# Kernel optimization log

Measured on AMD Instinct MI355X. Metric: run time of the kernel, lower is better.

Reference implementation:

```python
import jax, jax.numpy as jnp
import numpy as np

DIM = 1024
HEAD_DIM = 128
NUM_HEADS = 8
T = 8192
ATTN_SCALE = 0.1  # yarn.attn_scale after reset()
RMS_EPS = 1.1920929e-07  # torch F.rms_norm default eps for fp32


def setup_inputs() -> dict:
    key = jax.random.key(0)
    ks = jax.random.split(key, 6)
    x = jax.random.normal(ks[0], (1, T, DIM), jnp.float32)
    qkvo_w = jax.random.normal(ks[1], (4 * DIM, DIM), jnp.float32) * (DIM ** -0.5)
    ve = jax.random.normal(ks[2], (1, T, DIM), jnp.float32)
    sa_lambdas = jnp.array([0.9, 1.1], jnp.float32)
    attn_gate_w = jax.random.normal(ks[3], (NUM_HEADS, 12), jnp.float32) * 0.1
    ve_gate_w = jax.random.normal(ks[4], (NUM_HEADS, 12), jnp.float32) * 0.1
    # YaRN rotary factors, exactly as Yarn.reset()
    n_freq = HEAD_DIM // 4
    ang = (1.0 / 1024.0) ** jnp.linspace(0.0, 1.0, n_freq, dtype=jnp.float32)
    ang = jnp.repeat(ang, 2)                                   # [head_dim//2]
    ang = jnp.concatenate([ang, jnp.zeros(HEAD_DIM // 2, jnp.float32)])
    theta = jnp.arange(T, dtype=jnp.float32)[:, None] * ang[None, :]
    sign = jnp.where(jnp.arange(HEAD_DIM) % 2 == 1, -1.0, 1.0).astype(jnp.float32)
    factor1 = jnp.cos(theta)
    factor2 = jnp.sin(theta) * sign                            # odd lanes negated
    seqlens = jnp.array([0, 2048, 4096, 6144, 8192], jnp.int32)  # cu_seqlens
    return {"x": x, "qkvo_w": qkvo_w, "ve": ve, "sa_lambdas": sa_lambdas,
            "factor1": factor1, "factor2": factor2,
            "attn_gate_w": attn_gate_w, "ve_gate_w": ve_gate_w,
            "seqlens": seqlens, "bm_size": 128, "key_offset": 1}


def _rms_norm(x):
    return x * jax.lax.rsqrt(jnp.mean(x * x, axis=-1, keepdims=True) + RMS_EPS)


def _rotary(x, f1, f2):
    # x: [B, T, H, D]; pairwise flip of adjacent lanes, then f1*x + f2*flip(x)
    xf = x.reshape(*x.shape[:-1], x.shape[-1] // 2, 2)[..., ::-1].reshape(x.shape)
    return f1[None, :x.shape[1], None, :] * x + f2[None, :x.shape[1], None, :] * xf


def _windowed_varlen_attn(q, k, v, seqlens, bs, scale):
    # q,k,v: [T, H, D]; causal sliding window (bs left, 0 right), varlen via cu_seqlens.
    Tt, H, D = q.shape
    nb = Tt // bs
    pad = jnp.zeros((bs, H, D), q.dtype)
    kp = jnp.concatenate([pad, k], axis=0)
    vp = jnp.concatenate([pad, v], axis=0)
    idx = jnp.arange(nb)[:, None] * bs + jnp.arange(2 * bs)[None, :]   # [nb, 2bs] into padded
    kb, vb = kp[idx], vp[idx]                                          # [nb, 2bs, H, D]
    qb = q.reshape(nb, bs, H, D)
    gq = jnp.arange(Tt).reshape(nb, bs)                                # global query idx
    gk = idx - bs                                                      # global key idx (may be <0)
    seg = jnp.searchsorted(seqlens, jnp.arange(Tt), side='right')      # segment id per token
    sq = seg.reshape(nb, bs)
    sk = seg[jnp.clip(gk, 0, Tt - 1)]
    mask = ((gk[:, None, :] >= 0)
            & (gk[:, None, :] <= gq[:, :, None])
            & (gq[:, :, None] - gk[:, None, :] <= bs)
            & (sq[:, :, None] == sk[:, None, :]))                      # [nb, bs, 2bs]
    s = jnp.einsum('nqhd,nkhd->nhqk', qb, kb) * scale
    s = jnp.where(mask[:, None], s, -jnp.inf)
    p = jax.nn.softmax(s, axis=-1)
    return jnp.einsum('nhqk,nkhd->nqhd', p, vb).reshape(Tt, H, D)


def _forward(x, qkvo_w, ve, sa_lambdas, factor1, factor2, attn_gate_w, ve_gate_w,
             seqlens, bm_size, key_offset):
    B, Tt = x.shape[0], x.shape[1]
    H, D = NUM_HEADS, HEAD_DIM
    qkv = x @ (sa_lambdas[0] * qkvo_w[:3 * DIM]).T                    # [B, T, 3*dim]
    qkv = qkv.reshape(B, Tt, 3 * H, D)
    q, k, v = qkv[:, :, :H], qkv[:, :, H:2 * H], qkv[:, :, 2 * H:]
    q, k = _rms_norm(q), _rms_norm(k)
    q, k = _rotary(q, factor1, factor2), _rotary(k, factor1, factor2)
    if key_offset:
        hd2 = D // 2
        k_hi = jnp.concatenate([k[:, :1, :, hd2:], k[:, :-1, :, hd2:]], axis=1)
        k = jnp.concatenate([k[..., :hd2], k_hi], axis=-1)
    ve_gate = 2.0 * jax.nn.sigmoid(x[..., :12] @ ve_gate_w.T).reshape(B, Tt, H, 1)
    v = v + ve_gate * ve.reshape(B, Tt, H, D)
    y = _windowed_varlen_attn(q[0], k[0], v[0], seqlens, bm_size, ATTN_SCALE)
    y = y.reshape(B, Tt, H, D)
    y = y * jax.nn.sigmoid(x[..., :12] @ attn_gate_w.T).reshape(B, Tt, H, 1)
    y = y.reshape(B, Tt, H * D)
    return y @ (sa_lambdas[1] * qkvo_w[3 * DIM:]).T


def reference(x, qkvo_w, ve, sa_lambdas, factor1, factor2, attn_gate_w, ve_gate_w,
              seqlens, bm_size, key_offset):
    return _forward(x, qkvo_w, ve, sa_lambdas, factor1, factor2,
                    attn_gate_w, ve_gate_w, seqlens, bm_size, key_offset)
```

## Files before the change

### kernel.cpp

```cpp
#include <hip/hip_runtime.h>


#define TSEQ 8192
#define DIMM 1024
#define NHEAD 8
#define HD 128
#define ATTN_SCALE 0.1f
#define RMS_EPS 1.1920929e-07f

typedef __bf16 bfx2 __attribute__((ext_vector_type(2)));
typedef __bf16 bfx4 __attribute__((ext_vector_type(4)));
typedef __bf16 bfx8 __attribute__((ext_vector_type(8)));
typedef float f32x4 __attribute__((ext_vector_type(4)));
typedef short s16x4 __attribute__((ext_vector_type(4)));

#define GLDS16(g, l)                                                         \
  __builtin_amdgcn_global_load_lds(                                          \
      (const __attribute__((address_space(1))) void*)(g),                    \
      (__attribute__((address_space(3))) void*)(l), 16, 0, 0)

__device__ __forceinline__ float sig_(float z) { return 1.0f / (1.0f + __expf(-z)); }

__global__ void k_prep(const float4* __restrict__ x, const float4* __restrict__ w,
                       const float* __restrict__ lam, bfx4* __restrict__ xb,
                       bfx4* __restrict__ w1b, bfx4* __restrict__ w2b) {
  const int nx = TSEQ * DIMM / 4;
  const int nw = 4096 * 1024 / 4;
  const float l0 = lam[0], l1 = lam[1];
  int i = blockIdx.x * blockDim.x + threadIdx.x;
  int stride = gridDim.x * blockDim.x;
  for (; i < nx + nw; i += stride) {
    if (i < nx) {
      float4 v = x[i];
      bfx4 o;
      o[0] = (__bf16)v.x; o[1] = (__bf16)v.y; o[2] = (__bf16)v.z; o[3] = (__bf16)v.w;
      xb[i] = o;
    } else {
      int j = i - nx;
      int row = (j * 4) >> 10;
      float s = (row < 3 * DIMM) ? l0 : l1;
      float4 v = w[j];
      bfx4 o;
      o[0] = (__bf16)(s * v.x); o[1] = (__bf16)(s * v.y);
      o[2] = (__bf16)(s * v.z); o[3] = (__bf16)(s * v.w);
      if (row < 3 * DIMM) w1b[j] = o;
      else                w2b[j - 3 * DIMM * DIMM / 4] = o;
    }
  }
}

template <typename CT, int BK, int MINW>
__global__ __launch_bounds__(256, MINW) void k_gemm2b(const __bf16* __restrict__ A,
                                                      const __bf16* __restrict__ B,
                                                      CT* __restrict__ C,
                                                      int M, int N, int K) {
  constexpr int RB = BK * 2;
  constexpr int ABYTES = 128 * RB;
  constexpr int ROUNDS = ABYTES / 4096;
  __shared__ __align__(16) char ldsb[2][2 * ABYTES];
  const int tid = threadIdx.x;
  const int wave = tid >> 6, lane = tid & 63;
  const int wm = wave >> 1, wn = wave & 1;
  const int lr = lane & 15, lg = lane >> 4;
  const int bm = blockIdx.x, bn = blockIdx.y;

  const int slq  = (BK == 64) ? (tid & 7) : (tid & 3);
  const int srow = (BK == 64) ? (tid >> 3) : (tid >> 2);
  const int sswz = (BK == 64) ? (srow & 7) : ((srow >> 1) & 3);
  const int scol = (slq ^ sswz) * 8;
  const __bf16* Ag = A + (size_t)(bm * 128 + srow) * K + scol;
  const __bf16* Bg = B + (size_t)(bn * 128 + srow) * K + scol;

  char* buf0 = (char*)&ldsb[0][0];
  char* buf1 = (char*)&ldsb[1][0];

  auto stage = [&](int kt, char* buf) {
#pragma unroll
    for (int L = 0; L < ROUNDS; L++)
      GLDS16(Ag + (size_t)(L * (4096 / RB)) * K + kt * BK,
             buf + L * 4096 + wave * 1024);
#pragma unroll
    for (int L = 0; L < ROUNDS; L++)
      GLDS16(Bg + (size_t)(L * (4096 / RB)) * K + kt * BK,
             buf + ABYTES + L * 4096 + wave * 1024);
  };

  const int aoffs = (wm * 64 + lr) * RB;
  const int boffs = ABYTES + (wn * 64 + lr) * RB;
  const int rswz = (BK == 64) ? (lr & 7) : ((lr >> 1) & 3);
  const int s0 = (lg ^ rswz) * 16;
  const int s1 = ((4 + lg) ^ rswz) * 16;

  f32x4 acc[4][4] = {};

#define VMC0() asm volatile("s_waitcnt vmcnt(0)" ::: "memory")
#define BAR() __builtin_amdgcn_s_barrier()

  stage(0, buf0);
  VMC0(); BAR();

  const int NT = K / BK;
  for (int t = 0; t < NT; t++) {
    char* cur = (t & 1) ? buf1 : buf0;
    char* nxt = (t & 1) ? buf0 : buf1;
    if (t + 1 < NT) stage(t + 1, nxt);
    bfx8 af[4][2], bfr[4][2];
#pragma unroll
    for (int f = 0; f < 4; f++) {
      const char* p = cur + aoffs + f * 16 * RB;
      af[f][0] = *(const bfx8*)(p + s0);
      if constexpr (BK == 64) af[f][1] = *(const bfx8*)(p + s1);
    }
#pragma unroll
    for (int f = 0; f < 4; f++) {
      const char* p = cur + boffs + f * 16 * RB;
      bfr[f][0] = *(const bfx8*)(p + s0);
      if constexpr (BK == 64) bfr[f][1] = *(const bfx8*)(p + s1);
    }
    __builtin_amdgcn_s_setprio(1);
#pragma unroll
    for (int i = 0; i < 4; i++)
#pragma unroll
      for (int j = 0; j < 4; j++) {
        acc[i][j] = __builtin_amdgcn_mfma_f32_16x16x32_bf16(af[i][0], bfr[j][0], acc[i][j], 0, 0, 0);
        if constexpr (BK == 64)
          acc[i][j] = __builtin_amdgcn_mfma_f32_16x16x32_bf16(af[i][1], bfr[j][1], acc[i][j], 0, 0, 0);
      }
    __builtin_amdgcn_s_setprio(0);
    VMC0(); BAR();
  }

  const int rbase = bm * 128 + wm * 64 + lg * 4;
  const int cbase = bn * 128 + wn * 64 + lr;
#pragma unroll
  for (int f = 0; f < 4; f++)
#pragma unroll
    for (int rr = 0; rr < 4; rr++) {
      size_t rowoff = (size_t)(rbase + f * 16 + rr) * N + cbase;
#pragma unroll
      for (int nf = 0; nf < 4; nf++) C[rowoff + nf * 16] = (CT)acc[f][nf][rr];
    }
#undef VMC0
#undef BAR
}

__global__ __launch_bounds__(512) void k_qk(
    const __bf16* __restrict__ qkv, const float* __restrict__ f1,
    const float* __restrict__ f2, const int* __restrict__ koff_p,
    __bf16* __restrict__ qb, __bf16* __restrict__ kb) {
  const int t = blockIdx.x;
  const int h = threadIdx.x >> 6;
  const int l = threadIdx.x & 63;
  const int d0 = 2 * l;
  const size_t qoff = (size_t)t * (3 * DIMM) + h * HD;

  bfx2 qv = *(const bfx2*)&qkv[qoff + d0];
  bfx2 kv = *(const bfx2*)&qkv[qoff + DIMM + d0];
  float q0 = (float)qv[0], q1 = (float)qv[1];
  float k0 = (float)kv[0], k1 = (float)kv[1];

  float sq = q0 * q0 + q1 * q1;
  float sk = k0 * k0 + k1 * k1;
#pragma unroll
  for (int off = 32; off; off >>= 1) {
    sq += __shfl_xor(sq, off);
    sk += __shfl_xor(sk, off);
  }
  float rq = rsqrtf(sq * (1.0f / 128.0f) + RMS_EPS);
  float rk = rsqrtf(sk * (1.0f / 128.0f) + RMS_EPS);
  q0 *= rq; q1 *= rq; k0 *= rk; k1 *= rk;

  float2 cc = *(const float2*)&f1[(size_t)t * HD + d0];
  float2 ss = *(const float2*)&f2[(size_t)t * HD + d0];
  float rq0 = cc.x * q0 + ss.x * q1, rq1 = cc.y * q1 + ss.y * q0;
  float rk0 = cc.x * k0 + ss.x * k1, rk1 = cc.y * k1 + ss.y * k0;

  bfx2 qo; qo[0] = (__bf16)rq0; qo[1] = (__bf16)rq1;
  *(bfx2*)&qb[(size_t)t * DIMM + h * HD + d0] = qo;

  bfx2 ko2; ko2[0] = (__bf16)rk0; ko2[1] = (__bf16)rk1;
  const int koff = *koff_p;
  const size_t kcol = (size_t)h * HD + d0;
  if (!koff || l < 32) {
    *(bfx2*)&kb[(size_t)t * DIMM + kcol] = ko2;
  } else {
    if (t + 1 < TSEQ) *(bfx2*)&kb[(size_t)(t + 1) * DIMM + kcol] = ko2;
    if (t == 0)       *(bfx2*)&kb[kcol] = ko2;
  }
}

__global__ __launch_bounds__(512) void k_vgate(
    const __bf16* __restrict__ qkv, const float* __restrict__ x,
    const float* __restrict__ ve, const float* __restrict__ agw,
    const float* __restrict__ vgw, __bf16* __restrict__ vT,
    float* __restrict__ ag) {
  __shared__ float vg_lds[64][4];
  __shared__ __bf16 vtile[HD][68];
  const int t0 = blockIdx.x * 64;
  const int hbase = blockIdx.y * 4;
  const int tid = threadIdx.x;

  if (tid < 256) {
    const int tl = tid >> 2, hh = tid & 3;
    const int h = hbase + hh;
    const int t = t0 + tl;
    float za = 0.0f, zg = 0.0f;
#pragma unroll
    for (int j = 0; j < 12; j++) {
      float xv = x[(size_t)t * DIMM + j];
      za += xv * agw[h * 12 + j];
      zg += xv * vgw[h * 12 + j];
    }
    ag[(size_t)t * NHEAD + h] = sig_(za);
    vg_lds[tl][hh] = 2.0f * sig_(zg);
  }
  __syncthreads();

  const int w = tid >> 6, l = tid & 63;
  const int dout = tid >> 2, tof = (tid & 3) * 16;
  for (int hh = 0; hh < 4; hh++) {
    const int h = hbase + hh;
#pragma unroll
    for (int it = 0; it < 8; it++) {
      const int tl = w * 8 + it;
      const int t = t0 + tl;
      const size_t voff = (size_t)t * (3 * DIMM) + 2 * DIMM + h * HD;
      float va = (float)qkv[voff + l];
      float vb = (float)qkv[voff + l + 64];
      float vea = ve[(size_t)t * DIMM + h * HD + l];
      float veb = ve[(size_t)t * DIMM + h * HD + l + 64];
      float gv = vg_lds[tl][hh];
      vtile[l][tl]      = (__bf16)(va + gv * vea);
      vtile[l + 64][tl] = (__bf16)(vb + gv * veb);
    }
    __syncthreads();
    {
      bfx4 a0 = *(const bfx4*)&vtile[dout][tof];
      bfx4 a1 = *(const bfx4*)&vtile[dout][tof + 4];
      bfx4 a2 = *(const bfx4*)&vtile[dout][tof + 8];
      bfx4 a3 = *(const bfx4*)&vtile[dout][tof + 12];
      bfx8 p0, p1;
      p0[0]=a0[0]; p0[1]=a0[1]; p0[2]=a0[2]; p0[3]=a0[3];
      p0[4]=a1[0]; p0[5]=a1[1]; p0[6]=a1[2]; p0[7]=a1[3];
      p1[0]=a2[0]; p1[1]=a2[1]; p1[2]=a2[2]; p1[3]=a2[3];
      p1[4]=a3[0]; p1[5]=a3[1]; p1[6]=a3[2]; p1[7]=a3[3];
      __bf16* dst = &vT[(size_t)(h * HD + dout) * TSEQ + t0 + tof];
      *(bfx8*)dst = p0;
      *(bfx8*)(dst + 8) = p1;
    }
    __syncthreads();
  }
}

__global__ __launch_bounds__(512, 1) void k_attn3(
    const __bf16* __restrict__ qb, const __bf16* __restrict__ kb,
    const __bf16* __restrict__ vT, const float* __restrict__ ag,
    const int* __restrict__ sl, int ns, __bf16* __restrict__ yb) {
  __shared__ __align__(16) char kls[65536];
  __shared__ __align__(16) char vls[65536];
  const int n = blockIdx.x, h = blockIdx.y;
  const int tid = threadIdx.x;
  const int w = tid >> 6, l = tid & 63;
  const int lr = l & 15, lg = l >> 4;
  const int q0r = n * 128 + w * 16;
  const int kbase = q0r - 128;
  const int kbb = n * 128 - 128;
  const int q = q0r + lr;
  const int kfs = (q0r < 128) ? ((128 - q0r) >> 4) : 0;

  bfx8 qf[4];
#pragma unroll
  for (int ds = 0; ds < 4; ds++)
    qf[ds] = *(const bfx8*)&qb[(size_t)q * DIMM + h * HD + ds * 32 + lg * 8];

  {
    const int rr_ = tid >> 4;
    const int slot = tid & 15;
#pragma unroll
    for (int r = 0; r < 8; r++) {
      const int rel = r * 32 + rr_;
      int grow = kbb + rel;
      grow = grow < 0 ? 0 : grow;
      const int slotp = slot ^ (rel & 15);
      GLDS16(kb + (size_t)grow * DIMM + h * HD + slotp * 8,
             kls + r * 8192 + w * 1024);
    }
  }
  {
    const int slot = l & 31;
#pragma unroll
    for (int r = 0; r < 8; r++) {
      const int d = r * 16 + w * 2 + (l >> 5);
      const int slotp = slot ^ (d & 15);
      int tsrc = kbb + slotp * 8;
      tsrc = tsrc < 0 ? 0 : tsrc;
      GLDS16(vT + (size_t)(h * HD + d) * TSEQ + tsrc,
             vls + r * 8192 + w * 1024);
    }
  }

  int segs = 0;
  for (int i = 0; i < ns; i++) {
    int v = sl[i];
    segs = (v <= q) ? ((v > segs) ? v : segs) : segs;
  }
  int klo = q - 128;
  if (segs > klo) klo = segs;
  if (klo < 0) klo = 0;

  asm volatile("s_waitcnt vmcnt(0)" ::: "memory");
  __builtin_amdgcn_s_barrier();

  const int kswz = lr << 4;
  f32x4 sf[9] = {};
#pragma unroll
  for (int kf = 0; kf < 9; kf++) {
    if (kf >= kfs) {
      const int relrow = w * 16 + kf * 16 + lr;
      const char* kp = kls + relrow * 256;
      bfx8 k0 = *(const bfx8*)(kp + ((lg * 16) ^ kswz));
      bfx8 k1 = *(const bfx8*)(kp + ((64 + lg * 16) ^ kswz));
      bfx8 k2 = *(const bfx8*)(kp + ((128 + lg * 16) ^ kswz));
      bfx8 k3 = *(const bfx8*)(kp + ((192 + lg * 16) ^ kswz));
      sf[kf] = __builtin_amdgcn_mfma_f32_16x16x32_bf16(k0, qf[0], sf[kf], 0, 0, 0);
      sf[kf] = __builtin_amdgcn_mfma_f32_16x16x32_bf16(k1, qf[1], sf[kf], 0, 0, 0);
      sf[kf] = __builtin_amdgcn_mfma_f32_16x16x32_bf16(k2, qf[2], sf[kf], 0, 0, 0);
      sf[kf] = __builtin_amdgcn_mfma_f32_16x16x32_bf16(k3, qf[3], sf[kf], 0, 0, 0);
    }
  }

#pragma unroll
  for (int kf = 0; kf < 9; kf++)
#pragma unroll
    for (int rr = 0; rr < 4; rr++) {
      int k = kbase + kf * 16 + lg * 4 + rr;
      bool valid = (k >= klo) && (k <= q);
      sf[kf][rr] = valid ? sf[kf][rr] * ATTN_SCALE : -1e30f;
    }

  float mx = -1e30f;
#pragma unroll
  for (int kf = 0; kf < 9; kf++)
#pragma unroll
    for (int rr = 0; rr < 4; rr++) mx = fmaxf(mx, sf[kf][rr]);
  mx = fmaxf(mx, __shfl_xor(mx, 16));
  mx = fmaxf(mx, __shfl_xor(mx, 32));

  float lsum = 0.0f;
#pragma unroll
  for (int kf = 0; kf < 9; kf++)
#pragma unroll
    for (int rr = 0; rr < 4; rr++) {
      float p = __expf(sf[kf][rr] - mx);
      sf[kf][rr] = p;
      lsum += p;
    }
  lsum += __shfl_xor(lsum, 16);
  lsum += __shfl_xor(lsum, 32);

  f32x4 o[8] = {};
#pragma unroll
  for (int kf = 0; kf < 9; kf++) {
    if (kf >= kfs) {
      bfx4 pc;
      pc[0] = (__bf16)sf[kf][0]; pc[1] = (__bf16)sf[kf][1];
      pc[2] = (__bf16)sf[kf][2]; pc[3] = (__bf16)sf[kf][3];
      s16x4 pb = *(s16x4*)&pc;
      const int tof = (w * 32 + kf * 32 + lg * 8) ^ kswz;
#pragma unroll
      for (int nf = 0; nf < 8; nf++) {
        s16x4 vf = *(const s16x4*)(vls + (nf * 16 + lr) * 512 + tof);
        o[nf] = __builtin_amdgcn_mfma_f32_16x16x16bf16_1k(vf, pb, o[nf], 0, 0, 0);
      }
    }
  }

  const float sc = ag[(size_t)q * NHEAD + h] / lsum;
#pragma unroll
  for (int nf = 0; nf < 8; nf++) {
    bfx4 st;
#pragma unroll
    for (int rr = 0; rr < 4; rr++) st[rr] = (__bf16)(o[nf][rr] * sc);
    *(bfx4*)&yb[(size_t)q * DIMM + h * HD + nf * 16 + lg * 4] = st;
  }
}

extern "C" void kernel_launch(void* const* d_in, const int* in_sizes, int n_in,
                              void* d_out, int out_size, void* d_ws, size_t ws_size,
                              hipStream_t stream) {
  const float* x   = (const float*)d_in[0];
  const float* qw  = (const float*)d_in[1];
  const float* ve  = (const float*)d_in[2];
  const float* lam = (const float*)d_in[3];
  const float* f1  = (const float*)d_in[4];
  const float* f2  = (const float*)d_in[5];
  const float* agw = (const float*)d_in[6];
  const float* vgw = (const float*)d_in[7];
  const int*   sl  = (const int*)d_in[8];
  const int    ns  = in_sizes[8];
  const int*   koff = (const int*)d_in[10];
  float* out = (float*)d_out;
  char* ws = (char*)d_ws;

  const size_t MB = 1024 * 1024;
  if (ws_size < 105 * MB) return;
  __bf16* xb   = (__bf16*)(ws);
  __bf16* w1b  = (__bf16*)(ws + 16 * MB);
  __bf16* w2b  = (__bf16*)(ws + 22 * MB);
  __bf16* qkvb = (__bf16*)(ws + 24 * MB);
  __bf16* qbuf = (__bf16*)(ws + 72 * MB);
  __bf16* kbuf = (__bf16*)(ws + 88 * MB);
  float*  ag   = (float*)(ws + 104 * MB);
  __bf16* vT   = xb;
  __bf16* ybuf = qkvb;

  k_prep<<<3072, 256, 0, stream>>>((const float4*)x, (const float4*)qw, lam,
                                   (bfx4*)xb, (bfx4*)w1b, (bfx4*)w2b);
  k_gemm2b<__bf16, 32, 4><<<dim3(TSEQ / 128, 3 * DIMM / 128), 256, 0, stream>>>(
      xb, w1b, qkvb, TSEQ, 3 * DIMM, DIMM);
  k_qk<<<TSEQ, 512, 0, stream>>>(qkvb, f1, f2, koff, qbuf, kbuf);
  k_vgate<<<dim3(TSEQ / 64, 2), 512, 0, stream>>>(qkvb, x, ve, agw, vgw, vT, ag);
  k_attn3<<<dim3(TSEQ / 128, NHEAD), 512, 0, stream>>>(qbuf, kbuf, vT, ag, sl, ns, ybuf);
  k_gemm2b<float, 64, 2><<<dim3(TSEQ / 128, DIMM / 128), 256, 0, stream>>>(
      ybuf, w2b, out, TSEQ, DIMM, DIMM);
}
```

Measured before the change: 150.0 us.

## Fuse q/k norm-rotary and v-gate kernels; use BK=64 GEMM for QKV projection

Merges the per-token q/k RMS-norm plus rotary kernel and the v-gating/transpose kernel into one kernel that handles 32 tokens across all 8 heads. This saves a launch and lets the gate sigmoids be computed once per token block. The GEMM template is fixed to BK=64 with two waves per SIMD, so the QKV projection now also uses the larger K tile with fewer barriers. The trade-off is lower occupancy for that GEMM and fewer, heavier blocks for the post-processing step.

```diff
diff --git a/kernel.cpp b/kernel.cpp
--- a/kernel.cpp
+++ b/kernel.cpp
@@ -49,25 +49,20 @@
   }
 }
 
-template <typename CT, int BK, int MINW>
-__global__ __launch_bounds__(256, MINW) void k_gemm2b(const __bf16* __restrict__ A,
-                                                      const __bf16* __restrict__ B,
-                                                      CT* __restrict__ C,
-                                                      int M, int N, int K) {
-  constexpr int RB = BK * 2;
-  constexpr int ABYTES = 128 * RB;
-  constexpr int ROUNDS = ABYTES / 4096;
-  __shared__ __align__(16) char ldsb[2][2 * ABYTES];
+template <typename CT>
+__global__ __launch_bounds__(256, 2) void k_gemm2b(const __bf16* __restrict__ A,
+                                                   const __bf16* __restrict__ B,
+                                                   CT* __restrict__ C,
+                                                   int M, int N, int K) {
+  __shared__ __align__(16) __bf16 ldsb[2][256 * 64];
   const int tid = threadIdx.x;
   const int wave = tid >> 6, lane = tid & 63;
   const int wm = wave >> 1, wn = wave & 1;
   const int lr = lane & 15, lg = lane >> 4;
   const int bm = blockIdx.x, bn = blockIdx.y;
 
-  const int slq  = (BK == 64) ? (tid & 7) : (tid & 3);
-  const int srow = (BK == 64) ? (tid >> 3) : (tid >> 2);
-  const int sswz = (BK == 64) ? (srow & 7) : ((srow >> 1) & 3);
-  const int scol = (slq ^ sswz) * 8;
+  const int srow = tid >> 3;
+  const int scol = ((tid & 7) ^ (srow & 7)) * 8;
   const __bf16* Ag = A + (size_t)(bm * 128 + srow) * K + scol;
   const __bf16* Bg = B + (size_t)(bn * 128 + srow) * K + scol;
 
@@ -76,20 +71,17 @@
 
   auto stage = [&](int kt, char* buf) {
 #pragma unroll
-    for (int L = 0; L < ROUNDS; L++)
-      GLDS16(Ag + (size_t)(L * (4096 / RB)) * K + kt * BK,
-             buf + L * 4096 + wave * 1024);
-#pragma unroll
-    for (int L = 0; L < ROUNDS; L++)
-      GLDS16(Bg + (size_t)(L * (4096 / RB)) * K + kt * BK,
-             buf + ABYTES + L * 4096 + wave * 1024);
+    for (int L = 0; L < 4; L++)
+      GLDS16(Ag + (size_t)(L * 32) * K + kt * 64, buf + L * 4096 + wave * 1024);
+#pragma unroll
+    for (int L = 0; L < 4; L++)
+      GLDS16(Bg + (size_t)(L * 32) * K + kt * 64, buf + 16384 + L * 4096 + wave * 1024);
   };
 
-  const int aoffs = (wm * 64 + lr) * RB;
-  const int boffs = ABYTES + (wn * 64 + lr) * RB;
-  const int rswz = (BK == 64) ? (lr & 7) : ((lr >> 1) & 3);
-  const int s0 = (lg ^ rswz) * 16;
-  const int s1 = ((4 + lg) ^ rswz) * 16;
+  const int aoffs = (wm * 64 + lr) * 128;
+  const int boffs = 16384 + (wn * 64 + lr) * 128;
+  const int s0 = (lg ^ (lr & 7)) * 16;
+  const int s1 = ((4 + lg) ^ (lr & 7)) * 16;
 
   f32x4 acc[4][4] = {};
 
@@ -99,7 +91,7 @@
   stage(0, buf0);
   VMC0(); BAR();
 
-  const int NT = K / BK;
+  const int NT = K / 64;
   for (int t = 0; t < NT; t++) {
     char* cur = (t & 1) ? buf1 : buf0;
     char* nxt = (t & 1) ? buf0 : buf1;
@@ -107,15 +99,15 @@
     bfx8 af[4][2], bfr[4][2];
 #pragma unroll
     for (int f = 0; f < 4; f++) {
-      const char* p = cur + aoffs + f * 16 * RB;
+      const char* p = cur + aoffs + f * 2048;
       af[f][0] = *(const bfx8*)(p + s0);
-      if constexpr (BK == 64) af[f][1] = *(const bfx8*)(p + s1);
+      af[f][1] = *(const bfx8*)(p + s1);
     }
 #pragma unroll
     for (int f = 0; f < 4; f++) {
-      const char* p = cur + boffs + f * 16 * RB;
+      const char* p = cur + boffs + f * 2048;
       bfr[f][0] = *(const bfx8*)(p + s0);
-      if constexpr (BK == 64) bfr[f][1] = *(const bfx8*)(p + s1);
+      bfr[f][1] = *(const bfx8*)(p + s1);
     }
     __builtin_amdgcn_s_setprio(1);
 #pragma unroll
@@ -123,8 +115,7 @@
 #pragma unroll
       for (int j = 0; j < 4; j++) {
         acc[i][j] = __builtin_amdgcn_mfma_f32_16x16x32_bf16(af[i][0], bfr[j][0], acc[i][j], 0, 0, 0);
-        if constexpr (BK == 64)
-          acc[i][j] = __builtin_amdgcn_mfma_f32_16x16x32_bf16(af[i][1], bfr[j][1], acc[i][j], 0, 0, 0);
+        acc[i][j] = __builtin_amdgcn_mfma_f32_16x16x32_bf16(af[i][1], bfr[j][1], acc[i][j], 0, 0, 0);
       }
     __builtin_amdgcn_s_setprio(0);
     VMC0(); BAR();
@@ -144,91 +135,87 @@
 #undef BAR
 }
 
-__global__ __launch_bounds__(512) void k_qk(
-    const __bf16* __restrict__ qkv, const float* __restrict__ f1,
-    const float* __restrict__ f2, const int* __restrict__ koff_p,
-    __bf16* __restrict__ qb, __bf16* __restrict__ kb) {
-  const int t = blockIdx.x;
-  const int h = threadIdx.x >> 6;
-  const int l = threadIdx.x & 63;
+__global__ __launch_bounds__(512) void k_post(
+    const __bf16* __restrict__ qkv, const float* __restrict__ x,
+    const float* __restrict__ ve, const float* __restrict__ f1,
+    const float* __restrict__ f2, const float* __restrict__ agw,
+    const float* __restrict__ vgw, const int* __restrict__ koff_p,
+    __bf16* __restrict__ qb, __bf16* __restrict__ kb,
+    __bf16* __restrict__ vT, float* __restrict__ ag) {
+  __shared__ float vg_lds[32][8];
+  __shared__ __bf16 vtile[HD][36];
+  const int t0 = blockIdx.x * 32;
+  const int tid = threadIdx.x;
+  const int h = tid >> 6, l = tid & 63;
   const int d0 = 2 * l;
-  const size_t qoff = (size_t)t * (3 * DIMM) + h * HD;
-
-  bfx2 qv = *(const bfx2*)&qkv[qoff + d0];
-  bfx2 kv = *(const bfx2*)&qkv[qoff + DIMM + d0];
-  float q0 = (float)qv[0], q1 = (float)qv[1];
-  float k0 = (float)kv[0], k1 = (float)kv[1];
-
-  float sq = q0 * q0 + q1 * q1;
-  float sk = k0 * k0 + k1 * k1;
-#pragma unroll
-  for (int off = 32; off; off >>= 1) {
-    sq += __shfl_xor(sq, off);
-    sk += __shfl_xor(sk, off);
-  }
-  float rq = rsqrtf(sq * (1.0f / 128.0f) + RMS_EPS);
-  float rk = rsqrtf(sk * (1.0f / 128.0f) + RMS_EPS);
-  q0 *= rq; q1 *= rq; k0 *= rk; k1 *= rk;
-
-  float2 cc = *(const float2*)&f1[(size_t)t * HD + d0];
-  float2 ss = *(const float2*)&f2[(size_t)t * HD + d0];
-  float rq0 = cc.x * q0 + ss.x * q1, rq1 = cc.y * q1 + ss.y * q0;
-  float rk0 = cc.x * k0 + ss.x * k1, rk1 = cc.y * k1 + ss.y * k0;
-
-  bfx2 qo; qo[0] = (__bf16)rq0; qo[1] = (__bf16)rq1;
-  *(bfx2*)&qb[(size_t)t * DIMM + h * HD + d0] = qo;
-
-  bfx2 ko2; ko2[0] = (__bf16)rk0; ko2[1] = (__bf16)rk1;
   const int koff = *koff_p;
-  const size_t kcol = (size_t)h * HD + d0;
-  if (!koff || l < 32) {
-    *(bfx2*)&kb[(size_t)t * DIMM + kcol] = ko2;
-  } else {
-    if (t + 1 < TSEQ) *(bfx2*)&kb[(size_t)(t + 1) * DIMM + kcol] = ko2;
-    if (t == 0)       *(bfx2*)&kb[kcol] = ko2;
-  }
-}
-
-__global__ __launch_bounds__(512) void k_vgate(
-    const __bf16* __restrict__ qkv, const float* __restrict__ x,
-    const float* __restrict__ ve, const float* __restrict__ agw,
-    const float* __restrict__ vgw, __bf16* __restrict__ vT,
-    float* __restrict__ ag) {
-  __shared__ float vg_lds[64][4];
-  __shared__ __bf16 vtile[HD][68];
-  const int t0 = blockIdx.x * 64;
-  const int hbase = blockIdx.y * 4;
-  const int tid = threadIdx.x;
 
   if (tid < 256) {
-    const int tl = tid >> 2, hh = tid & 3;
-    const int h = hbase + hh;
+    const int tl = tid >> 3, hh = tid & 7;
     const int t = t0 + tl;
     float za = 0.0f, zg = 0.0f;
 #pragma unroll
     for (int j = 0; j < 12; j++) {
       float xv = x[(size_t)t * DIMM + j];
-      za += xv * agw[h * 12 + j];
-      zg += xv * vgw[h * 12 + j];
-    }
-    ag[(size_t)t * NHEAD + h] = sig_(za);
+      za += xv * agw[hh * 12 + j];
+      zg += xv * vgw[hh * 12 + j];
+    }
+    ag[(size_t)t * NHEAD + hh] = sig_(za);
     vg_lds[tl][hh] = 2.0f * sig_(zg);
   }
+
+#pragma unroll 2
+  for (int tl = 0; tl < 32; tl++) {
+    const int t = t0 + tl;
+    const size_t qoff = (size_t)t * (3 * DIMM) + h * HD;
+
+    bfx2 qv = *(const bfx2*)&qkv[qoff + d0];
+    bfx2 kv = *(const bfx2*)&qkv[qoff + DIMM + d0];
+    float q0 = (float)qv[0], q1 = (float)qv[1];
+    float k0 = (float)kv[0], k1 = (float)kv[1];
+
+    float sq = q0 * q0 + q1 * q1;
+    float sk = k0 * k0 + k1 * k1;
+#pragma unroll
+    for (int off = 32; off; off >>= 1) {
+      sq += __shfl_xor(sq, off);
+      sk += __shfl_xor(sk, off);
+    }
+    float rq = rsqrtf(sq * (1.0f / 128.0f) + RMS_EPS);
+    float rk = rsqrtf(sk * (1.0f / 128.0f) + RMS_EPS);
+    q0 *= rq; q1 *= rq; k0 *= rk; k1 *= rk;
+
+    float2 cc = *(const float2*)&f1[(size_t)t * HD + d0];
+    float2 ss = *(const float2*)&f2[(size_t)t * HD + d0];
+    float rq0 = cc.x * q0 + ss.x * q1, rq1 = cc.y * q1 + ss.y * q0;
+    float rk0 = cc.x * k0 + ss.x * k1, rk1 = cc.y * k1 + ss.y * k0;
+
+    bfx2 qo; qo[0] = (__bf16)rq0; qo[1] = (__bf16)rq1;
+    *(bfx2*)&qb[(size_t)t * DIMM + h * HD + d0] = qo;
+
+    bfx2 ko2; ko2[0] = (__bf16)rk0; ko2[1] = (__bf16)rk1;
+    const size_t kcol = (size_t)h * HD + d0;
+    if (!koff || l < 32) {
+      *(bfx2*)&kb[(size_t)t * DIMM + kcol] = ko2;
+    } else {
+      if (t + 1 < TSEQ) *(bfx2*)&kb[(size_t)(t + 1) * DIMM + kcol] = ko2;
+      if (t == 0)       *(bfx2*)&kb[kcol] = ko2;
+    }
+  }
   __syncthreads();
 
-  const int w = tid >> 6, l = tid & 63;
-  const int dout = tid >> 2, tof = (tid & 3) * 16;
-  for (int hh = 0; hh < 4; hh++) {
-    const int h = hbase + hh;
-#pragma unroll
-    for (int it = 0; it < 8; it++) {
-      const int tl = w * 8 + it;
+  const int w = tid >> 6;
+  const int dout = tid >> 2, tof = (tid & 3) * 8;
+  for (int hh = 0; hh < 8; hh++) {
+#pragma unroll
+    for (int it = 0; it < 4; it++) {
+      const int tl = w * 4 + it;
       const int t = t0 + tl;
-      const size_t voff = (size_t)t * (3 * DIMM) + 2 * DIMM + h * HD;
+      const size_t voff = (size_t)t * (3 * DIMM) + 2 * DIMM + hh * HD;
       float va = (float)qkv[voff + l];
       float vb = (float)qkv[voff + l + 64];
-      float vea = ve[(size_t)t * DIMM + h * HD + l];
-      float veb = ve[(size_t)t * DIMM + h * HD + l + 64];
+      float vea = ve[(size_t)t * DIMM + hh * HD + l];
+      float veb = ve[(size_t)t * DIMM + hh * HD + l + 64];
       float gv = vg_lds[tl][hh];
       vtile[l][tl]      = (__bf16)(va + gv * vea);
       vtile[l + 64][tl] = (__bf16)(vb + gv * veb);
@@ -237,16 +224,10 @@
     {
       bfx4 a0 = *(const bfx4*)&vtile[dout][tof];
       bfx4 a1 = *(const bfx4*)&vtile[dout][tof + 4];
-      bfx4 a2 = *(const bfx4*)&vtile[dout][tof + 8];
-      bfx4 a3 = *(const bfx4*)&vtile[dout][tof + 12];
-      bfx8 p0, p1;
-      p0[0]=a0[0]; p0[1]=a0[1]; p0[2]=a0[2]; p0[3]=a0[3];
-      p0[4]=a1[0]; p0[5]=a1[1]; p0[6]=a1[2]; p0[7]=a1[3];
-      p1[0]=a2[0]; p1[1]=a2[1]; p1[2]=a2[2]; p1[3]=a2[3];
-      p1[4]=a3[0]; p1[5]=a3[1]; p1[6]=a3[2]; p1[7]=a3[3];
-      __bf16* dst = &vT[(size_t)(h * HD + dout) * TSEQ + t0 + tof];
-      *(bfx8*)dst = p0;
-      *(bfx8*)(dst + 8) = p1;
+      bfx8 p0;
+      p0[0] = a0[0]; p0[1] = a0[1]; p0[2] = a0[2]; p0[3] = a0[3];
+      p0[4] = a1[0]; p0[5] = a1[1]; p0[6] = a1[2]; p0[7] = a1[3];
+      *(bfx8*)&vT[(size_t)(hh * HD + dout) * TSEQ + t0 + tof] = p0;
     }
     __syncthreads();
   }
@@ -416,11 +397,11 @@
 
   k_prep<<<3072, 256, 0, stream>>>((const float4*)x, (const float4*)qw, lam,
                                    (bfx4*)xb, (bfx4*)w1b, (bfx4*)w2b);
-  k_gemm2b<__bf16, 32, 4><<<dim3(TSEQ / 128, 3 * DIMM / 128), 256, 0, stream>>>(
+  k_gemm2b<__bf16><<<dim3(TSEQ / 128, 3 * DIMM / 128), 256, 0, stream>>>(
       xb, w1b, qkvb, TSEQ, 3 * DIMM, DIMM);
-  k_qk<<<TSEQ, 512, 0, stream>>>(qkvb, f1, f2, koff, qbuf, kbuf);
-  k_vgate<<<dim3(TSEQ / 64, 2), 512, 0, stream>>>(qkvb, x, ve, agw, vgw, vT, ag);
+  k_post<<<TSEQ / 32, 512, 0, stream>>>(qkvb, x, ve, f1, f2, agw, vgw, koff,
+                                        qbuf, kbuf, vT, ag);
   k_attn3<<<dim3(TSEQ / 128, NHEAD), 512, 0, stream>>>(qbuf, kbuf, vT, ag, sl, ns, ybuf);
-  k_gemm2b<float, 64, 2><<<dim3(TSEQ / 128, DIMM / 128), 256, 0, stream>>>(
+  k_gemm2b<float><<<dim3(TSEQ / 128, DIMM / 128), 256, 0, stream>>>(
       ybuf, w2b, out, TSEQ, DIMM, DIMM);
 }
```

After: 147.3 us. Within noise of the previous version (-1.8%).
